# Optimization experiments

Hardware: AMD Instinct MI355X
Metric: run time of the kernel (lower is better)

## Reference

```python
import jax, jax.numpy as jnp
import numpy as np

B = 1048576
N_BINS = 64
LOGIT_SCALE = 10.0  # cur_logit_scale default, detached in the original


def setup_inputs() -> dict:
    key = jax.random.key(0)
    k1, k2, k3 = jax.random.split(key, 3)
    y_hat = jax.random.normal(k1, (B, N_BINS), dtype=jnp.float32)
    t = jax.random.randint(k2, (B,), 0, N_BINS, dtype=jnp.int64)
    e = jax.random.randint(k3, (B,), 0, 2, dtype=jnp.int64)
    return {"y_hat": y_hat, "t": t, "e": e}


def reference(y_hat, t, e):
    # SurvEMD forward: p=2, raw_distance=True, reduction='mean'
    n_bins = y_hat.shape[-1]
    dt = y_hat.dtype
    t = t.reshape(-1, 1)
    e = e.reshape(-1, 1).astype(dt)  # binary censoring indicator as float
    j = jnp.arange(n_bins)  # bin index vector

    # convert_survival_label, vectorized:
    # target[i,j] = 1 at j==t[i]; plus (1-e[i]) for all j > t[i]
    onehot = (j == t).astype(dt)
    target = onehot + (1.0 - e) * (j > t).astype(dt)  # values in {0,1}

    target_dist = jax.nn.softmax((2.0 * target - 1.0) * LOGIT_SCALE, axis=-1)
    pred = (1.0 - e) * ((1.0 - target) * y_hat + target * LOGIT_SCALE) + e * y_hat
    pred_dist = jax.nn.softmax(pred, axis=-1)

    # cdf_loss with p=2, normalize_dist=False, ret_raw=True:
    d = jnp.cumsum(pred_dist, axis=-1) - jnp.cumsum(target_dist, axis=-1)
    loss = jnp.sum(d * d, axis=-1)  # [B]
    return loss.mean()
```

## Files before the change

kernel.cpp:

```cpp
#include <hip/hip_runtime.h>

#define NBINS 64

template <int CTRL>
__device__ __forceinline__ float dpp_shr_add(float x) {
    int xi = __float_as_int(x);
    int sh = __builtin_amdgcn_update_dpp(0, xi, CTRL, 0xF, 0xF, true);
    return x + __int_as_float(sh);
}

__device__ __forceinline__ float quad_rows(const float4* __restrict__ yv,
                                           const int* __restrict__ t,
                                           const int* __restrict__ e,
                                           int quad, int lane, int n_rows) {
    const int seg = lane >> 4;
    const int sl  = lane & 15;
    const int row = quad * 4 + seg;
    const bool valid = row < n_rows;
    const int crow = valid ? row : (n_rows - 1);

    const int tt = t[crow];
    const int ee = e[crow];
    const float4 y = yv[(size_t)crow * (NBINS / 4) + sl];

    const int j0 = sl * 4;

    const bool cen = (ee == 0);
    const float x0 = __expf((cen && (j0 + 0 >= tt)) ? 10.0f : y.x);
    const float x1 = __expf((cen && (j0 + 1 >= tt)) ? 10.0f : y.y);
    const float x2 = __expf((cen && (j0 + 2 >= tt)) ? 10.0f : y.z);
    const float x3 = __expf((cen && (j0 + 3 >= tt)) ? 10.0f : y.w);

    const float p0 = x0;
    const float p1 = p0 + x1;
    const float p2 = p1 + x2;
    const float p3 = p2 + x3;

    float sc = p3;
    sc = dpp_shr_add<0x111>(sc);
    sc = dpp_shr_add<0x112>(sc);
    sc = dpp_shr_add<0x114>(sc);
    sc = dpp_shr_add<0x118>(sc);

    const float total = __shfl(sc, 15, 16);
    const float excl  = sc - p3;
    const float rtot  = __builtin_amdgcn_rcpf(total);
    const float er    = excl * rtot;

    const float s = 2.0611536224385579e-9f;
    const float k  = (ee == 1) ? 1.0f : (float)(NBINS - tt);
    const float hi = __builtin_amdgcn_rcpf(k + (64.0f - k) * s);
    const float lo = s * hi;

    float acc = 0.0f;
    #pragma unroll
    for (int c = 0; c < 4; ++c) {
        const int j = j0 + c;
        const float p = (c == 0) ? p0 : (c == 1) ? p1 : (c == 2) ? p2 : p3;
        const float ones = (j >= tt) ? ((ee == 1) ? 1.0f : (float)(j - tt + 1))
                                     : 0.0f;
        const float cts = ones * hi + ((float)(j + 1) - ones) * lo;
        const float cps = fmaf(p, rtot, er);
        const float d = cps - cts;
        acc = fmaf(d, d, acc);
    }
    return valid ? acc : 0.0f;
}

__global__ __launch_bounds__(256) void survemd_kernel(
    const float* __restrict__ y_hat,
    const int* __restrict__ t,
    const int* __restrict__ e,
    float* __restrict__ out,
    int n_rows)
{
    const int lane = threadIdx.x & 63;
    const int wave_in_block = threadIdx.x >> 6;
    const int waves_per_block = blockDim.x >> 6;
    const int wave_id = blockIdx.x * waves_per_block + wave_in_block;
    const int total_waves = gridDim.x * waves_per_block;

    const float4* yv = (const float4*)y_hat;
    const int nquads = (n_rows + 3) >> 2;

    float acc = 0.0f;
    for (int q = wave_id; q < nquads; q += 2 * total_waves) {
        acc += quad_rows(yv, t, e, q, lane, n_rows);
        const int q2 = q + total_waves;
        if (q2 < nquads)
            acc += quad_rows(yv, t, e, q2, lane, n_rows);
    }

    #pragma unroll
    for (int off = 32; off >= 1; off >>= 1)
        acc += __shfl_down(acc, off, 64);

    __shared__ float wave_sums[8];
    if (lane == 0) wave_sums[wave_in_block] = acc;
    __syncthreads();
    if (threadIdx.x == 0) {
        float bsum = 0.0f;
        for (int w = 0; w < waves_per_block; ++w) bsum += wave_sums[w];
        atomicAdd(out, bsum * (1.0f / (float)n_rows));
    }
}

extern "C" void kernel_launch(void* const* d_in, const int* in_sizes, int n_in,
                              void* d_out, int out_size, void* d_ws, size_t ws_size,
                              hipStream_t stream) {
    const float* y_hat = (const float*)d_in[0];
    const int*   t     = (const int*)d_in[1];
    const int*   e     = (const int*)d_in[2];
    float* out = (float*)d_out;

    const int n_rows = in_sizes[1];

    (void)hipMemsetAsync(out, 0, out_size * sizeof(float), stream);

    const int block = 256;
    const int grid  = 8192;
    survemd_kernel<<<grid, block, 0, stream>>>(y_hat, t, e, out, n_rows);
}
```

Measured before the change: 405.8 us.

## Batch eight quad loads per wave up front and size grid to exact work

Replaces the grid-stride loop, which loaded two quads per iteration, with a fixed assignment of eight consecutive quads per wave. All eight sets of loads are issued before any computation to raise memory-level parallelism. The grid is now computed from the row count, so each wave runs once with no loop. This adds register pressure from holding eight float4 values plus t and e per lane, and launches many more blocks, which increases block launch and atomic reduction overhead.

```diff
diff --git a/kernel.cpp b/kernel.cpp
--- a/kernel.cpp
+++ b/kernel.cpp
@@ -9,20 +9,8 @@
     return x + __int_as_float(sh);
 }
 
-__device__ __forceinline__ float quad_rows(const float4* __restrict__ yv,
-                                           const int* __restrict__ t,
-                                           const int* __restrict__ e,
-                                           int quad, int lane, int n_rows) {
-    const int seg = lane >> 4;
-    const int sl  = lane & 15;
-    const int row = quad * 4 + seg;
-    const bool valid = row < n_rows;
-    const int crow = valid ? row : (n_rows - 1);
-
-    const int tt = t[crow];
-    const int ee = e[crow];
-    const float4 y = yv[(size_t)crow * (NBINS / 4) + sl];
-
+__device__ __forceinline__ float quad_compute(float4 y, int tt, int ee,
+                                              int sl, bool valid) {
     const int j0 = sl * 4;
 
     const bool cen = (ee == 0);
@@ -67,6 +55,8 @@
     return valid ? acc : 0.0f;
 }
 
+#define QUADS_PER_WAVE 8
+
 __global__ __launch_bounds__(256) void survemd_kernel(
     const float* __restrict__ y_hat,
     const int* __restrict__ t,
@@ -78,18 +68,32 @@
     const int wave_in_block = threadIdx.x >> 6;
     const int waves_per_block = blockDim.x >> 6;
     const int wave_id = blockIdx.x * waves_per_block + wave_in_block;
-    const int total_waves = gridDim.x * waves_per_block;
 
+    const int seg = lane >> 4;
+    const int sl  = lane & 15;
     const float4* yv = (const float4*)y_hat;
-    const int nquads = (n_rows + 3) >> 2;
+
+    const int base_quad = wave_id * QUADS_PER_WAVE;
+
+    float4 y[QUADS_PER_WAVE];
+    int    tt[QUADS_PER_WAVE];
+    int    ee[QUADS_PER_WAVE];
+    bool   valid[QUADS_PER_WAVE];
+    #pragma unroll
+    for (int u = 0; u < QUADS_PER_WAVE; ++u) {
+        const int row = (base_quad + u) * 4 + seg;
+        const bool v = row < n_rows;
+        const int crow = v ? row : (n_rows - 1);
+        y[u]  = yv[(size_t)crow * (NBINS / 4) + sl];
+        tt[u] = t[crow];
+        ee[u] = e[crow];
+        valid[u] = v;
+    }
 
     float acc = 0.0f;
-    for (int q = wave_id; q < nquads; q += 2 * total_waves) {
-        acc += quad_rows(yv, t, e, q, lane, n_rows);
-        const int q2 = q + total_waves;
-        if (q2 < nquads)
-            acc += quad_rows(yv, t, e, q2, lane, n_rows);
-    }
+    #pragma unroll
+    for (int u = 0; u < QUADS_PER_WAVE; ++u)
+        acc += quad_compute(y[u], tt[u], ee[u], sl, valid[u]);
 
     #pragma unroll
     for (int off = 32; off >= 1; off >>= 1)
@@ -117,7 +121,9 @@
 
     (void)hipMemsetAsync(out, 0, out_size * sizeof(float), stream);
 
-    const int block = 256;
-    const int grid  = 8192;
+    const int nquads = (n_rows + 3) >> 2;
+    const int waves  = (nquads + QUADS_PER_WAVE - 1) / QUADS_PER_WAVE;
+    const int block  = 256;
+    const int grid   = (waves + 3) / 4;
     survemd_kernel<<<grid, block, 0, stream>>>(y_hat, t, e, out, n_rows);
 }
```

Result: faster. 385.1 us (-5.1%).

## Software-pipeline chunked row loads with contiguous per-wave ranges and smaller grid

Applied to the files above, without the earlier changes.

Each wave now processes a contiguous range of chunks, where a chunk is 4 quads (16 rows). The next chunk's y/t/e loads are issued before the current chunk is computed, a register double buffer meant to hide memory latency. The target-CDF arithmetic is also simplified into fma form with a precomputed slope and offset. The grid shrinks to 2048 blocks and launch bounds request 4 blocks per CU. In exchange, register pressure from the buffered chunks goes up, and fewer waves are in flight.

```diff
diff --git a/kernel.cpp b/kernel.cpp
--- a/kernel.cpp
+++ b/kernel.cpp
@@ -1,6 +1,7 @@
 #include <hip/hip_runtime.h>
 
 #define NBINS 64
+#define QPC 4
 
 template <int CTRL>
 __device__ __forceinline__ float dpp_shr_add(float x) {
@@ -9,65 +10,86 @@
     return x + __int_as_float(sh);
 }
 
-__device__ __forceinline__ float quad_rows(const float4* __restrict__ yv,
+struct Chunk {
+    float4 y[QPC];
+    int    t[QPC];
+    int    e[QPC];
+};
+
+__device__ __forceinline__ void load_chunk(Chunk& c,
+                                           const float4* __restrict__ yv,
                                            const int* __restrict__ t,
                                            const int* __restrict__ e,
-                                           int quad, int lane, int n_rows) {
-    const int seg = lane >> 4;
-    const int sl  = lane & 15;
-    const int row = quad * 4 + seg;
-    const bool valid = row < n_rows;
-    const int crow = valid ? row : (n_rows - 1);
+                                           int chunk, int seg, int sl,
+                                           int n_rows) {
+    #pragma unroll
+    for (int u = 0; u < QPC; ++u) {
+        const int row = (chunk * QPC + u) * 4 + seg;
+        const int crow = min(row, n_rows - 1);
+        c.y[u] = yv[(size_t)crow * (NBINS / 4) + sl];
+        c.t[u] = t[crow];
+        c.e[u] = e[crow];
+    }
+}
 
-    const int tt = t[crow];
-    const int ee = e[crow];
-    const float4 y = yv[(size_t)crow * (NBINS / 4) + sl];
-
+__device__ __forceinline__ float compute_chunk(const Chunk& c, int chunk,
+                                               int seg, int sl, int n_rows) {
     const int j0 = sl * 4;
-
-    const bool cen = (ee == 0);
-    const float x0 = __expf((cen && (j0 + 0 >= tt)) ? 10.0f : y.x);
-    const float x1 = __expf((cen && (j0 + 1 >= tt)) ? 10.0f : y.y);
-    const float x2 = __expf((cen && (j0 + 2 >= tt)) ? 10.0f : y.z);
-    const float x3 = __expf((cen && (j0 + 3 >= tt)) ? 10.0f : y.w);
-
-    const float p0 = x0;
-    const float p1 = p0 + x1;
-    const float p2 = p1 + x2;
-    const float p3 = p2 + x3;
-
-    float sc = p3;
-    sc = dpp_shr_add<0x111>(sc);
-    sc = dpp_shr_add<0x112>(sc);
-    sc = dpp_shr_add<0x114>(sc);
-    sc = dpp_shr_add<0x118>(sc);
-
-    const float total = __shfl(sc, 15, 16);
-    const float excl  = sc - p3;
-    const float rtot  = __builtin_amdgcn_rcpf(total);
-    const float er    = excl * rtot;
-
-    const float s = 2.0611536224385579e-9f;
-    const float k  = (ee == 1) ? 1.0f : (float)(NBINS - tt);
-    const float hi = __builtin_amdgcn_rcpf(k + (64.0f - k) * s);
-    const float lo = s * hi;
-
     float acc = 0.0f;
     #pragma unroll
-    for (int c = 0; c < 4; ++c) {
-        const int j = j0 + c;
-        const float p = (c == 0) ? p0 : (c == 1) ? p1 : (c == 2) ? p2 : p3;
-        const float ones = (j >= tt) ? ((ee == 1) ? 1.0f : (float)(j - tt + 1))
-                                     : 0.0f;
-        const float cts = ones * hi + ((float)(j + 1) - ones) * lo;
-        const float cps = fmaf(p, rtot, er);
-        const float d = cps - cts;
-        acc = fmaf(d, d, acc);
+    for (int u = 0; u < QPC; ++u) {
+        const int row = (chunk * QPC + u) * 4 + seg;
+        const int tt = c.t[u];
+        const int ee = c.e[u];
+        const float4 y = c.y[u];
+
+        const bool cen = (ee == 0);
+        const float x0 = __expf((cen && (j0 + 0 >= tt)) ? 10.0f : y.x);
+        const float x1 = __expf((cen && (j0 + 1 >= tt)) ? 10.0f : y.y);
+        const float x2 = __expf((cen && (j0 + 2 >= tt)) ? 10.0f : y.z);
+        const float x3 = __expf((cen && (j0 + 3 >= tt)) ? 10.0f : y.w);
+
+        const float p0 = x0;
+        const float p1 = p0 + x1;
+        const float p2 = p1 + x2;
+        const float p3 = p2 + x3;
+
+        float sc = p3;
+        sc = dpp_shr_add<0x111>(sc);
+        sc = dpp_shr_add<0x112>(sc);
+        sc = dpp_shr_add<0x114>(sc);
+        sc = dpp_shr_add<0x118>(sc);
+
+        const float total = __shfl(sc, 15, 16);
+        const float excl  = sc - p3;
+        const float rtot  = __builtin_amdgcn_rcpf(total);
+        const float er    = excl * rtot;
+
+        const float s = 2.0611536224385579e-9f;
+        const float k  = (ee == 1) ? 1.0f : (float)(NBINS - tt);
+        const float hi = __builtin_amdgcn_rcpf(k + (64.0f - k) * s);
+        const float lo = s * hi;
+        const float hl = hi - lo;
+        const float slope = cen ? hl : 0.0f;
+        const float off   = cen ? (float)(1 - tt) * hl : hl;
+
+        float q = 0.0f;
+        #pragma unroll
+        for (int cc = 0; cc < 4; ++cc) {
+            const int j = j0 + cc;
+            const float p = (cc == 0) ? p0 : (cc == 1) ? p1
+                          : (cc == 2) ? p2 : p3;
+            const float m   = (j >= tt) ? fmaf((float)j, slope, off) : 0.0f;
+            const float cts = fmaf((float)(j + 1), lo, m);
+            const float d   = fmaf(p, rtot, er - cts);
+            q = fmaf(d, d, q);
+        }
+        acc += (row < n_rows) ? q : 0.0f;
     }
-    return valid ? acc : 0.0f;
+    return acc;
 }
 
-__global__ __launch_bounds__(256) void survemd_kernel(
+__global__ __launch_bounds__(256, 4) void survemd_kernel(
     const float* __restrict__ y_hat,
     const int* __restrict__ t,
     const int* __restrict__ e,
@@ -80,15 +102,28 @@
     const int wave_id = blockIdx.x * waves_per_block + wave_in_block;
     const int total_waves = gridDim.x * waves_per_block;
 
+    const int seg = lane >> 4;
+    const int sl  = lane & 15;
     const float4* yv = (const float4*)y_hat;
-    const int nquads = (n_rows + 3) >> 2;
+
+    const int nquads  = (n_rows + 3) >> 2;
+    const int nchunks = (nquads + QPC - 1) / QPC;
+    const int cpw     = (nchunks + total_waves - 1) / total_waves;
+
+    const int begin = wave_id * cpw;
+    const int end   = min(begin + cpw, nchunks);
 
     float acc = 0.0f;
-    for (int q = wave_id; q < nquads; q += 2 * total_waves) {
-        acc += quad_rows(yv, t, e, q, lane, n_rows);
-        const int q2 = q + total_waves;
-        if (q2 < nquads)
-            acc += quad_rows(yv, t, e, q2, lane, n_rows);
+    if (begin < end) {
+        Chunk A;
+        load_chunk(A, yv, t, e, begin, seg, sl, n_rows);
+        for (int i = begin; i < end; ++i) {
+            Chunk B;
+            const int nxt = (i + 1 < end) ? i + 1 : i;
+            load_chunk(B, yv, t, e, nxt, seg, sl, n_rows);
+            acc += compute_chunk(A, i, seg, sl, n_rows);
+            A = B;
+        }
     }
 
     #pragma unroll
@@ -118,6 +153,6 @@
     (void)hipMemsetAsync(out, 0, out_size * sizeof(float), stream);
 
     const int block = 256;
-    const int grid  = 8192;
+    const int grid  = 2048;
     survemd_kernel<<<grid, block, 0, stream>>>(y_hat, t, e, out, n_rows);
 }
```

After: 374.3 us. 7.7% less time.
